# Optimization experiments

Measured on AMD Instinct MI355X. Metric: run time of the kernel, lower is better.

Reference implementation:

```python
import jax, jax.numpy as jnp
import numpy as np

NEG_SLOPE = 0.2


def _gather_neighbour(pc, idx):
    # pc: (B, N, d), idx: (B, N, k) -> (B, N, k, d)
    B, N, d = pc.shape
    k = idx.shape[-1]
    flat = idx.reshape(B, N * k)[..., None]            # (B, N*k, 1)
    g = jnp.take_along_axis(pc, flat, axis=1)          # (B, N*k, d)
    return g.reshape(B, N, k, d)


def _block(x, idx, W2, g2, b2, W1, g1, b1):
    # gather -> 1x1 conv (BN folded, ReLU) -> max/mean over k -> concat -> 1x1 conv (BN folded, no act)
    g = _gather_neighbour(x, idx)                      # (B, N, k, d)
    h = jax.nn.relu(jnp.einsum('bnkd,de->bnke', g, W2) * g2 + b2)
    mx = h.max(axis=2)                                 # (B, N, d_out)
    mn = h.mean(axis=2)                                # (B, N, d_out)
    cat = jnp.concatenate([mx, mn], axis=-1)           # (B, N, 2*d_out)
    return jnp.einsum('bnc,cd->bnd', cat, W1) * g1 + b1


def setup_inputs() -> dict:
    key = jax.random.key(0)
    ks = jax.random.split(key, 8)
    B, N, K, D = 2, 65536, 16, 32
    x = jax.random.normal(ks[0], (B, N, D), dtype=jnp.float32)
    idx = jax.random.randint(ks[1], (B, N, K), 0, N, dtype=jnp.int32)
    L = 4  # four stacked blocks
    W2d = jax.random.normal(ks[2], (L, D, D), dtype=jnp.float32) * 0.05
    gamma2 = jnp.ones((L, 1, 1, 1, D), dtype=jnp.float32)
    beta2 = jax.random.normal(ks[3], (L, 1, 1, 1, D), dtype=jnp.float32) * 0.01
    W1d = jax.random.normal(ks[4], (L, 2 * D, D), dtype=jnp.float32) * 0.05
    gamma1 = jnp.ones((L, 1, 1, D), dtype=jnp.float32)
    beta1 = jax.random.normal(ks[5], (L, 1, 1, D), dtype=jnp.float32) * 0.01
    return {"x": x, "idx": idx, "W2d": W2d, "gamma2": gamma2, "beta2": beta2,
            "W1d": W1d, "gamma1": gamma1, "beta1": beta1}


def reference(x, idx, W2d, gamma2, beta2, W1d, gamma1, beta1):
    lrelu = lambda v: jax.nn.leaky_relu(v, NEG_SLOPE)
    blk = lambda inp, i: _block(inp, idx, W2d[i], gamma2[i][0], beta2[i][0],
                                W1d[i], gamma1[i][0], beta1[i][0])
    x1 = blk(x, 0)
    tmp = lrelu(x1)
    x2 = blk(tmp, 1)
    tmp = lrelu(x2 + x1)
    x3 = blk(tmp, 2)
    tmp = lrelu(x3 + x2)
    x4 = blk(tmp, 3)
    return lrelu(x1 + x2 + x3 + x4)
```

## Files before the change

### kernel.cpp

```cpp
#include <hip/hip_runtime.h>
#include <hip/hip_fp16.h>

namespace {

typedef _Float16 half8 __attribute__((ext_vector_type(8)));
typedef float f32x4 __attribute__((ext_vector_type(4)));

constexpr int kN = 65536;
constexpr int kD = 32;
constexpr int kPts = 2 * kN;
constexpr int kThreads = 256;
constexpr int kPtsPerBlk = 64;
constexpr int kBlocks = kPts / kPtsPerBlk;
constexpr int kNumFrags = 24;
static_assert(kBlocks * kPtsPerBlk == kPts, "grid must tile points exactly");
static_assert(kN % kPtsPerBlk == 0, "blocks must not straddle batch boundary");

__device__ __forceinline__ float relu_(float v) { return fmaxf(v, 0.f); }
__device__ __forceinline__ float lrelu_(float v) { return v >= 0.f ? v : 0.2f * v; }

__device__ __forceinline__ int pi_(int k) {
    const int c = ((k >> 3) << 2) + ((k & 7) >> 1);
    return (k & 1) ? c + 16 : c;
}

__global__ __launch_bounds__(kThreads)
void pack_kernel(const float* __restrict__ W2d, const float* __restrict__ W1d,
                 uint4* __restrict__ wpack)
{
    for (int id = threadIdx.x; id < kNumFrags * 64; id += kThreads) {
        const int fid = id >> 6, l = id & 63, n = l & 15, q = l >> 4;
        half8 v;
        if (fid < 2) {
            const int h = fid;
#pragma unroll
            for (int j = 0; j < 8; ++j)
                v[j] = (_Float16)W2d[(q * 8 + j) * kD + h * 16 + n];
        } else {
            const int rel = fid - 2;
            const int layer = (rel < 18) ? rel / 6 : 3;
            const int sub   = (rel < 18) ? rel % 6 : rel - 18;
            if (sub < 4) {
                const int p = sub >> 1, h = sub & 1;
#pragma unroll
                for (int j = 0; j < 8; ++j)
                    v[j] = (_Float16)W1d[layer * 2048 + (p * 32 + pi_(q * 8 + j)) * kD + h * 16 + n];
            } else {
                const int h = sub - 4;
#pragma unroll
                for (int j = 0; j < 8; ++j)
                    v[j] = (_Float16)W2d[(layer + 1) * 1024 + pi_(q * 8 + j) * kD + h * 16 + n];
            }
        }
        wpack[id] = *reinterpret_cast<const uint4*>(&v);
    }
}

__global__ __launch_bounds__(kThreads, 4)
void zprep_kernel(const float* __restrict__ x, const int4* __restrict__ idx4,
                  const uint4* __restrict__ wfrag,
                  const float* __restrict__ g2v, const float* __restrict__ b2v,
                  __half2* __restrict__ z, uint2* __restrict__ idx16)
{
    const int tid  = threadIdx.x;
    {
        const int p = blockIdx.x * kPtsPerBlk + (tid >> 2);
        const int part = tid & 3;
        const int4 iv = idx4[p * 4 + part];
        uint2 o;
        o.x = (unsigned)(iv.x & 0xFFFF) | ((unsigned)iv.y << 16);
        o.y = (unsigned)(iv.z & 0xFFFF) | ((unsigned)iv.w << 16);
        idx16[p * 4 + part] = o;
    }
    const int w    = tid >> 6;
    const int lane = tid & 63;
    const int n    = lane & 15;
    const int q    = lane >> 4;
    const int pbase = blockIdx.x * kPtsPerBlk + w * 16;
    const int point = pbase + n;

    const float4 x0 = reinterpret_cast<const float4*>(x)[point * 8 + q * 2];
    const float4 x1 = reinterpret_cast<const float4*>(x)[point * 8 + q * 2 + 1];
    half8 ax;
    ax[0] = (_Float16)x0.x; ax[1] = (_Float16)x0.y;
    ax[2] = (_Float16)x0.z; ax[3] = (_Float16)x0.w;
    ax[4] = (_Float16)x1.x; ax[5] = (_Float16)x1.y;
    ax[6] = (_Float16)x1.z; ax[7] = (_Float16)x1.w;

    const uint4 u0 = wfrag[0 * 64 + lane];
    const uint4 u1 = wfrag[1 * 64 + lane];
    const half8 b0 = *reinterpret_cast<const half8*>(&u0);
    const half8 b1 = *reinterpret_cast<const half8*>(&u1);
    f32x4 a0 = {0.f, 0.f, 0.f, 0.f}, a1 = {0.f, 0.f, 0.f, 0.f};
    a0 = __builtin_amdgcn_mfma_f32_16x16x32_f16(ax, b0, a0, 0, 0, 0);
    a1 = __builtin_amdgcn_mfma_f32_16x16x32_f16(ax, b1, a1, 0, 0, 0);

    const float g20 = g2v[n], g21 = g2v[16 + n];
    const float c20 = b2v[n], c21 = b2v[16 + n];
#pragma unroll
    for (int r = 0; r < 4; ++r) {
        const int pm = pbase + q * 4 + r;
        z[pm * 16 + n] = __floats2half2_rn(relu_(fmaf(a0[r], g20, c20)),
                                           relu_(fmaf(a1[r], g21, c21)));
    }
}

template <int MODE>
__global__ __launch_bounds__(kThreads, 4)
void blk_kernel(const uint4* __restrict__ zsrc, const uint4* __restrict__ idx16,
                const uint4* __restrict__ wfrag,
                const float* __restrict__ g1v, const float* __restrict__ b1v,
                const float* __restrict__ g2v, const float* __restrict__ b2v,
                const uint4* __restrict__ prev, uint4* __restrict__ cur,
                float* __restrict__ sacc, __half2* __restrict__ znext)
{
    __shared__ float2 tb[4][16][17];

    const int tid  = threadIdx.x;
    const int w    = tid >> 6;
    const int lane = tid & 63;
    const int n    = lane & 15;
    const int q    = lane >> 4;
    const int pbase = blockIdx.x * kPtsPerBlk + w * 16;
    const int point = pbase + n;
    const int base  = pbase & ~(kN - 1);

    const uint4 iv0 = idx16[point * 2 + 0];
    const uint4 iv1 = idx16[point * 2 + 1];

    const uint4 f0 = wfrag[0 * 64 + lane];
    const uint4 f1 = wfrag[1 * 64 + lane];
    const uint4 f2 = wfrag[2 * 64 + lane];
    const uint4 f3 = wfrag[3 * 64 + lane];
    const half8 bA0 = *reinterpret_cast<const half8*>(&f0);
    const half8 bA1 = *reinterpret_cast<const half8*>(&f1);
    const half8 bB0 = *reinterpret_cast<const half8*>(&f2);
    const half8 bB1 = *reinterpret_cast<const half8*>(&f3);

    float mx[8], sm[8];
#pragma unroll
    for (int c = 0; c < 8; ++c) { mx[c] = 0.f; sm[c] = 0.f; }
    const unsigned* ivw = reinterpret_cast<const unsigned*>(&iv0);
#pragma unroll
    for (int k = 0; k < 16; ++k) {
        unsigned word;
        if (k < 8) word = reinterpret_cast<const unsigned*>(&iv0)[k >> 1];
        else       word = reinterpret_cast<const unsigned*>(&iv1)[(k - 8) >> 1];
        const int row = (k & 1) ? (int)(word >> 16) : (int)(word & 0xFFFFu);
        const uint4 u = zsrc[(base + row) * 4 + q];
        const __half2* h = reinterpret_cast<const __half2*>(&u);
#pragma unroll
        for (int c = 0; c < 4; ++c) {
            const float2 f = __half22float2(h[c]);
            mx[2 * c]     = fmaxf(mx[2 * c], f.x);     sm[2 * c]     += f.x;
            mx[2 * c + 1] = fmaxf(mx[2 * c + 1], f.y); sm[2 * c + 1] += f.y;
        }
    }
    (void)ivw;
    half8 amax, amean;
#pragma unroll
    for (int c = 0; c < 8; ++c) {
        amax[c]  = (_Float16)mx[c];
        amean[c] = (_Float16)(sm[c] * 0.0625f);
    }

    f32x4 acc0 = {0.f, 0.f, 0.f, 0.f}, acc1 = {0.f, 0.f, 0.f, 0.f};
    acc0 = __builtin_amdgcn_mfma_f32_16x16x32_f16(amax,  bA0, acc0, 0, 0, 0);
    acc0 = __builtin_amdgcn_mfma_f32_16x16x32_f16(amean, bB0, acc0, 0, 0, 0);
    acc1 = __builtin_amdgcn_mfma_f32_16x16x32_f16(amax,  bA1, acc1, 0, 0, 0);
    acc1 = __builtin_amdgcn_mfma_f32_16x16x32_f16(amean, bB1, acc1, 0, 0, 0);

    const float g10 = g1v[n], g11 = g1v[16 + n];
    const float c10 = b1v[n], c11 = b1v[16 + n];
#pragma unroll
    for (int r = 0; r < 4; ++r) {
        tb[w][q * 4 + r][n] = make_float2(fmaf(acc0[r], g10, c10),
                                          fmaf(acc1[r], g11, c11));
    }
    __builtin_amdgcn_wave_barrier();
    float y8[8];
#pragma unroll
    for (int s = 0; s < 4; ++s) {
        const float2 f = tb[w][n][q * 4 + s];
        y8[2 * s] = f.x; y8[2 * s + 1] = f.y;
    }

    const int sb0 = point * kD + q * 4;
    const int sb1 = sb0 + 16;
    float t8[8];
    if (MODE == 0) {
        reinterpret_cast<float4*>(sacc)[sb0 >> 2] = make_float4(y8[0], y8[2], y8[4], y8[6]);
        reinterpret_cast<float4*>(sacc)[sb1 >> 2] = make_float4(y8[1], y8[3], y8[5], y8[7]);
        half8 ch;
#pragma unroll
        for (int c = 0; c < 8; ++c) ch[c] = (_Float16)y8[c];
        cur[point * 4 + q] = *reinterpret_cast<const uint4*>(&ch);
#pragma unroll
        for (int c = 0; c < 8; ++c) t8[c] = lrelu_(y8[c]);
    } else if (MODE == 1 || MODE == 2) {
        float4 s0 = reinterpret_cast<const float4*>(sacc)[sb0 >> 2];
        float4 s1 = reinterpret_cast<const float4*>(sacc)[sb1 >> 2];
        s0.x += y8[0]; s0.y += y8[2]; s0.z += y8[4]; s0.w += y8[6];
        s1.x += y8[1]; s1.y += y8[3]; s1.z += y8[5]; s1.w += y8[7];
        reinterpret_cast<float4*>(sacc)[sb0 >> 2] = s0;
        reinterpret_cast<float4*>(sacc)[sb1 >> 2] = s1;
        const uint4 pv = prev[point * 4 + q];
        const __half2* ph = reinterpret_cast<const __half2*>(&pv);
#pragma unroll
        for (int c = 0; c < 4; ++c) {
            const float2 f = __half22float2(ph[c]);
            t8[2 * c]     = lrelu_(y8[2 * c] + f.x);
            t8[2 * c + 1] = lrelu_(y8[2 * c + 1] + f.y);
        }
        if (MODE == 1) {
            half8 ch;
#pragma unroll
            for (int c = 0; c < 8; ++c) ch[c] = (_Float16)y8[c];
            cur[point * 4 + q] = *reinterpret_cast<const uint4*>(&ch);
        }
    } else {
        const float4 s0 = reinterpret_cast<const float4*>(sacc)[sb0 >> 2];
        const float4 s1 = reinterpret_cast<const float4*>(sacc)[sb1 >> 2];
        reinterpret_cast<float4*>(sacc)[sb0 >> 2] =
            make_float4(lrelu_(s0.x + y8[0]), lrelu_(s0.y + y8[2]),
                        lrelu_(s0.z + y8[4]), lrelu_(s0.w + y8[6]));
        reinterpret_cast<float4*>(sacc)[sb1 >> 2] =
            make_float4(lrelu_(s1.x + y8[1]), lrelu_(s1.y + y8[3]),
                        lrelu_(s1.z + y8[5]), lrelu_(s1.w + y8[7]));
        return;
    }

    half8 at;
#pragma unroll
    for (int c = 0; c < 8; ++c) at[c] = (_Float16)t8[c];
    const uint4 f4 = wfrag[4 * 64 + lane];
    const uint4 f5 = wfrag[5 * 64 + lane];
    const half8 bz0 = *reinterpret_cast<const half8*>(&f4);
    const half8 bz1 = *reinterpret_cast<const half8*>(&f5);
    f32x4 az0 = {0.f, 0.f, 0.f, 0.f}, az1 = {0.f, 0.f, 0.f, 0.f};
    az0 = __builtin_amdgcn_mfma_f32_16x16x32_f16(at, bz0, az0, 0, 0, 0);
    az1 = __builtin_amdgcn_mfma_f32_16x16x32_f16(at, bz1, az1, 0, 0, 0);

    const float g20 = g2v[n], g21 = g2v[16 + n];
    const float c20 = b2v[n], c21 = b2v[16 + n];
#pragma unroll
    for (int r = 0; r < 4; ++r) {
        const int pm = pbase + q * 4 + r;
        znext[pm * 16 + n] = __floats2half2_rn(relu_(fmaf(az0[r], g20, c20)),
                                               relu_(fmaf(az1[r], g21, c21)));
    }
}

}

extern "C" void kernel_launch(void* const* d_in, const int* in_sizes, int n_in,
                              void* d_out, int out_size, void* d_ws, size_t ws_size,
                              hipStream_t stream)
{
    const float* x   = (const float*)d_in[0];
    const int4*  idx = (const int4*)d_in[1];
    const float* W2d = (const float*)d_in[2];
    const float* g2  = (const float*)d_in[3];
    const float* b2  = (const float*)d_in[4];
    const float* W1d = (const float*)d_in[5];
    const float* g1  = (const float*)d_in[6];
    const float* b1  = (const float*)d_in[7];
    float* out = (float*)d_out;
    char*  ws  = (char*)d_ws;

    constexpr size_t kHalfMap = (size_t)kPts * kD * sizeof(__half);
    __half2* zA = (__half2*)(ws);
    __half2* zB = (__half2*)(ws + kHalfMap);
    uint4*   cA = (uint4*)(ws + 2 * kHalfMap);
    uint4*   cB = (uint4*)(ws + 3 * kHalfMap);
    uint2*   idx16 = (uint2*)(ws + 4 * kHalfMap);
    uint4*   wpack = (uint4*)(ws + 4 * kHalfMap + (size_t)kPts * 32);

    const dim3 grid(kBlocks), blk(kThreads);
    pack_kernel<<<dim3(1), blk, 0, stream>>>(W2d, W1d, wpack);
    zprep_kernel<<<grid, blk, 0, stream>>>(x, idx, wpack, g2, b2, zA, idx16);

    const uint4* i16 = (const uint4*)idx16;
    blk_kernel<0><<<grid, blk, 0, stream>>>((const uint4*)zA, i16,
        wpack + (2 + 0 * 6) * 64, g1, b1, g2 + 1 * kD, b2 + 1 * kD,
        nullptr, cA, out, zB);
    blk_kernel<1><<<grid, blk, 0, stream>>>((const uint4*)zB, i16,
        wpack + (2 + 1 * 6) * 64, g1 + 1 * kD, b1 + 1 * kD, g2 + 2 * kD, b2 + 2 * kD,
        cA, cB, out, zA);
    blk_kernel<2><<<grid, blk, 0, stream>>>((const uint4*)zA, i16,
        wpack + (2 + 2 * 6) * 64, g1 + 2 * kD, b1 + 2 * kD, g2 + 3 * kD, b2 + 3 * kD,
        cB, nullptr, out, zB);
    blk_kernel<3><<<grid, blk, 0, stream>>>((const uint4*)zB, i16,
        wpack + (2 + 3 * 6) * 64, g1 + 3 * kD, b1 + 3 * kD, nullptr, nullptr,
        nullptr, nullptr, out, nullptr);
}
```

Baseline: 186.7 us.

## Fold weight packing into zprep and remap gather lanes for coalesced neighbour loads

Removes the separate single-block pack kernel launch by having block 0 of zprep build the packed fragments, while every zprep block loads its first-layer weights directly from W2d. In blk_kernel, each group of four lanes now gathers one point's full 64-byte feature row instead of the MFMA fragment lane mapping. The per-point max/mean results are staged through shared memory and reloaded in MFMA layout. This aims to make the gathers more contiguous and to cut a launch, at the cost of extra LDS traffic and a wave barrier.

```diff
diff --git a/kernel.cpp b/kernel.cpp
--- a/kernel.cpp
+++ b/kernel.cpp
@@ -24,45 +24,42 @@
     return (k & 1) ? c + 16 : c;
 }
 
-__global__ __launch_bounds__(kThreads)
-void pack_kernel(const float* __restrict__ W2d, const float* __restrict__ W1d,
-                 uint4* __restrict__ wpack)
-{
-    for (int id = threadIdx.x; id < kNumFrags * 64; id += kThreads) {
-        const int fid = id >> 6, l = id & 63, n = l & 15, q = l >> 4;
-        half8 v;
-        if (fid < 2) {
-            const int h = fid;
-#pragma unroll
-            for (int j = 0; j < 8; ++j)
-                v[j] = (_Float16)W2d[(q * 8 + j) * kD + h * 16 + n];
-        } else {
-            const int rel = fid - 2;
-            const int layer = (rel < 18) ? rel / 6 : 3;
-            const int sub   = (rel < 18) ? rel % 6 : rel - 18;
-            if (sub < 4) {
-                const int p = sub >> 1, h = sub & 1;
-#pragma unroll
-                for (int j = 0; j < 8; ++j)
-                    v[j] = (_Float16)W1d[layer * 2048 + (p * 32 + pi_(q * 8 + j)) * kD + h * 16 + n];
-            } else {
-                const int h = sub - 4;
-#pragma unroll
-                for (int j = 0; j < 8; ++j)
-                    v[j] = (_Float16)W2d[(layer + 1) * 1024 + pi_(q * 8 + j) * kD + h * 16 + n];
-            }
-        }
-        wpack[id] = *reinterpret_cast<const uint4*>(&v);
-    }
-}
-
 __global__ __launch_bounds__(kThreads, 4)
 void zprep_kernel(const float* __restrict__ x, const int4* __restrict__ idx4,
-                  const uint4* __restrict__ wfrag,
+                  const float* __restrict__ W2d, const float* __restrict__ W1d,
                   const float* __restrict__ g2v, const float* __restrict__ b2v,
-                  __half2* __restrict__ z, uint2* __restrict__ idx16)
+                  __half2* __restrict__ z, uint2* __restrict__ idx16,
+                  uint4* __restrict__ wpack)
 {
-    const int tid  = threadIdx.x;
+    const int tid = threadIdx.x;
+    if (blockIdx.x == 0) {
+        for (int id = tid; id < kNumFrags * 64; id += kThreads) {
+            const int fid = id >> 6, l = id & 63, n = l & 15, q = l >> 4;
+            half8 v;
+            if (fid < 2) {
+                const int h = fid;
+#pragma unroll
+                for (int j = 0; j < 8; ++j)
+                    v[j] = (_Float16)W2d[(q * 8 + j) * kD + h * 16 + n];
+            } else {
+                const int rel = fid - 2;
+                const int layer = (rel < 18) ? rel / 6 : 3;
+                const int sub   = (rel < 18) ? rel % 6 : rel - 18;
+                if (sub < 4) {
+                    const int p = sub >> 1, h = sub & 1;
+#pragma unroll
+                    for (int j = 0; j < 8; ++j)
+                        v[j] = (_Float16)W1d[layer * 2048 + (p * 32 + pi_(q * 8 + j)) * kD + h * 16 + n];
+                } else {
+                    const int h = sub - 4;
+#pragma unroll
+                    for (int j = 0; j < 8; ++j)
+                        v[j] = (_Float16)W2d[(layer + 1) * 1024 + pi_(q * 8 + j) * kD + h * 16 + n];
+                }
+            }
+            wpack[id] = *reinterpret_cast<const uint4*>(&v);
+        }
+    }
     {
         const int p = blockIdx.x * kPtsPerBlk + (tid >> 2);
         const int part = tid & 3;
@@ -87,10 +84,12 @@
     ax[4] = (_Float16)x1.x; ax[5] = (_Float16)x1.y;
     ax[6] = (_Float16)x1.z; ax[7] = (_Float16)x1.w;
 
-    const uint4 u0 = wfrag[0 * 64 + lane];
-    const uint4 u1 = wfrag[1 * 64 + lane];
-    const half8 b0 = *reinterpret_cast<const half8*>(&u0);
-    const half8 b1 = *reinterpret_cast<const half8*>(&u1);
+    half8 b0, b1;
+#pragma unroll
+    for (int j = 0; j < 8; ++j) {
+        b0[j] = (_Float16)W2d[(q * 8 + j) * kD + n];
+        b1[j] = (_Float16)W2d[(q * 8 + j) * kD + 16 + n];
+    }
     f32x4 a0 = {0.f, 0.f, 0.f, 0.f}, a1 = {0.f, 0.f, 0.f, 0.f};
     a0 = __builtin_amdgcn_mfma_f32_16x16x32_f16(ax, b0, a0, 0, 0, 0);
     a1 = __builtin_amdgcn_mfma_f32_16x16x32_f16(ax, b1, a1, 0, 0, 0);
@@ -114,6 +113,8 @@
                 const uint4* __restrict__ prev, uint4* __restrict__ cur,
                 float* __restrict__ sacc, __half2* __restrict__ znext)
 {
+    __shared__ __align__(16) _Float16 gmax[4][16][40];
+    __shared__ __align__(16) _Float16 gmean[4][16][40];
     __shared__ float2 tb[4][16][17];
 
     const int tid  = threadIdx.x;
@@ -125,8 +126,44 @@
     const int point = pbase + n;
     const int base  = pbase & ~(kN - 1);
 
-    const uint4 iv0 = idx16[point * 2 + 0];
-    const uint4 iv1 = idx16[point * 2 + 1];
+    const int gpt = lane >> 2;
+    const int gq  = lane & 3;
+    const int gpoint = pbase + gpt;
+    const uint4 iv0 = idx16[gpoint * 2 + 0];
+    const uint4 iv1 = idx16[gpoint * 2 + 1];
+
+    float mx[8], sm[8];
+#pragma unroll
+    for (int c = 0; c < 8; ++c) { mx[c] = 0.f; sm[c] = 0.f; }
+#pragma unroll
+    for (int k = 0; k < 16; ++k) {
+        unsigned word;
+        if (k < 8) word = reinterpret_cast<const unsigned*>(&iv0)[k >> 1];
+        else       word = reinterpret_cast<const unsigned*>(&iv1)[(k - 8) >> 1];
+        const int row = (k & 1) ? (int)(word >> 16) : (int)(word & 0xFFFFu);
+        const uint4 u = zsrc[(base + row) * 4 + gq];
+        const __half2* h = reinterpret_cast<const __half2*>(&u);
+#pragma unroll
+        for (int c = 0; c < 4; ++c) {
+            const float2 f = __half22float2(h[c]);
+            mx[2 * c]     = fmaxf(mx[2 * c], f.x);     sm[2 * c]     += f.x;
+            mx[2 * c + 1] = fmaxf(mx[2 * c + 1], f.y); sm[2 * c + 1] += f.y;
+        }
+    }
+    {
+        half8 hmx, hmn;
+#pragma unroll
+        for (int c = 0; c < 8; ++c) {
+            hmx[c] = (_Float16)mx[c];
+            hmn[c] = (_Float16)(sm[c] * 0.0625f);
+        }
+        *reinterpret_cast<half8*>(&gmax[w][gpt][gq * 8])  = hmx;
+        *reinterpret_cast<half8*>(&gmean[w][gpt][gq * 8]) = hmn;
+    }
+    __builtin_amdgcn_wave_barrier();
+
+    const half8 amax  = *reinterpret_cast<const half8*>(&gmax[w][n][q * 8]);
+    const half8 amean = *reinterpret_cast<const half8*>(&gmean[w][n][q * 8]);
 
     const uint4 f0 = wfrag[0 * 64 + lane];
     const uint4 f1 = wfrag[1 * 64 + lane];
@@ -136,33 +173,6 @@
     const half8 bA1 = *reinterpret_cast<const half8*>(&f1);
     const half8 bB0 = *reinterpret_cast<const half8*>(&f2);
     const half8 bB1 = *reinterpret_cast<const half8*>(&f3);
-
-    float mx[8], sm[8];
-#pragma unroll
-    for (int c = 0; c < 8; ++c) { mx[c] = 0.f; sm[c] = 0.f; }
-    const unsigned* ivw = reinterpret_cast<const unsigned*>(&iv0);
-#pragma unroll
-    for (int k = 0; k < 16; ++k) {
-        unsigned word;
-        if (k < 8) word = reinterpret_cast<const unsigned*>(&iv0)[k >> 1];
-        else       word = reinterpret_cast<const unsigned*>(&iv1)[(k - 8) >> 1];
-        const int row = (k & 1) ? (int)(word >> 16) : (int)(word & 0xFFFFu);
-        const uint4 u = zsrc[(base + row) * 4 + q];
-        const __half2* h = reinterpret_cast<const __half2*>(&u);
-#pragma unroll
-        for (int c = 0; c < 4; ++c) {
-            const float2 f = __half22float2(h[c]);
-            mx[2 * c]     = fmaxf(mx[2 * c], f.x);     sm[2 * c]     += f.x;
-            mx[2 * c + 1] = fmaxf(mx[2 * c + 1], f.y); sm[2 * c + 1] += f.y;
-        }
-    }
-    (void)ivw;
-    half8 amax, amean;
-#pragma unroll
-    for (int c = 0; c < 8; ++c) {
-        amax[c]  = (_Float16)mx[c];
-        amean[c] = (_Float16)(sm[c] * 0.0625f);
-    }
 
     f32x4 acc0 = {0.f, 0.f, 0.f, 0.f}, acc1 = {0.f, 0.f, 0.f, 0.f};
     acc0 = __builtin_amdgcn_mfma_f32_16x16x32_f16(amax,  bA0, acc0, 0, 0, 0);
@@ -277,8 +287,8 @@
     uint4*   wpack = (uint4*)(ws + 4 * kHalfMap + (size_t)kPts * 32);
 
     const dim3 grid(kBlocks), blk(kThreads);
-    pack_kernel<<<dim3(1), blk, 0, stream>>>(W2d, W1d, wpack);
-    zprep_kernel<<<grid, blk, 0, stream>>>(x, idx, wpack, g2, b2, zA, idx16);
+    zprep_kernel<<<grid, blk, 0, stream>>>(x, idx, W2d, W1d, g2, b2,
+                                           zA, idx16, wpack);
 
     const uint4* i16 = (const uint4*)idx16;
     blk_kernel<0><<<grid, blk, 0, stream>>>((const uint4*)zA, i16,
```

Result: faster. 180.1 us (-3.5%).
